# Kernel tuning notes

Measured on AMD Instinct MI355X. Metric: run time of the kernel, lower is better.

Reference implementation:

```python
import jax, jax.numpy as jnp
import numpy as np

N = 100000      # nodes
E = 1600000     # edges
G = 256         # graphs in batch
D_IN = 92
D = 64          # out_dim
EPS = 1e-5      # batchnorm eps


def setup_inputs() -> dict:
    key = jax.random.key(0)
    ks = jax.random.split(key, 20)

    def lin_w(k, fan_in, fan_out):
        return jax.random.normal(k, (fan_in, fan_out), jnp.float32) / np.sqrt(fan_in).astype(np.float32)

    inp = {
        "x": jax.random.normal(ks[0], (N, D_IN), jnp.float32),
        "edge_index": jax.random.randint(ks[1], (2, E), 0, N, dtype=jnp.int64),
        "edge_weight": jax.random.uniform(ks[2], (E,), jnp.float32),
        "batch": jnp.sort(jax.random.randint(ks[3], (N,), 0, G, dtype=jnp.int64)),
        # GCNConv layer 0 (in_channels -> out_dim) + BatchNorm
        "W0": lin_w(ks[4], D_IN, D), "b0": jnp.zeros((D,), jnp.float32),
        "g0": jnp.ones((D,), jnp.float32), "beta0": jnp.zeros((D,), jnp.float32),
        # GCNConv layers 1,2 (out_dim -> out_dim) + BatchNorms
        "W1": lin_w(ks[5], D, D), "b1": jnp.zeros((D,), jnp.float32),
        "g1": jnp.ones((D,), jnp.float32), "beta1": jnp.zeros((D,), jnp.float32),
        "W2": lin_w(ks[6], D, D), "b2": jnp.zeros((D,), jnp.float32),
        "g2": jnp.ones((D,), jnp.float32), "beta2": jnp.zeros((D,), jnp.float32),
        # post MLP: Linear(out_dim,100) -> ReLU -> Linear(100,1)
        "Wp1": lin_w(ks[7], D, 100), "bp1": jnp.zeros((100,), jnp.float32),
        "Wp2": lin_w(ks[8], 100, 1), "bp2": jnp.zeros((1,), jnp.float32),
    }
    return inp


def reference(x, edge_index, edge_weight, batch,
              W0, b0, g0, beta0,
              W1, b1, g1, beta1,
              W2, b2, g2, beta2,
              Wp1, bp1, Wp2, bp2):
    n = x.shape[0]
    # --- gcn_norm with self-loops (fill weight 1), symmetric normalization ---
    loop = jnp.arange(n)
    row = jnp.concatenate([edge_index[0], loop])          # source nodes
    col = jnp.concatenate([edge_index[1], loop])          # target nodes
    w = jnp.concatenate([edge_weight, jnp.ones((n,), x.dtype)])
    deg = jax.ops.segment_sum(w, col, num_segments=n)
    dinv = jnp.where(deg > 0, deg ** -0.5, 0.0)
    norm = dinv[row] * w * dinv[col]                      # [E+N]

    def conv(h, W, b):
        h = h @ W                                         # [n, D]
        msg = norm[:, None] * h[row]                      # gather + scale
        return jax.ops.segment_sum(msg, col, num_segments=n) + b

    def bn(h, g, beta):  # training-mode batchnorm over node dim
        mu = h.mean(0)
        var = h.var(0)
        return (h - mu) * jax.lax.rsqrt(var + EPS) * g + beta

    h = jax.nn.relu(bn(conv(x, W0, b0), g0, beta0))
    h = jax.nn.relu(bn(conv(h, W1, b1), g1, beta1))
    h = jax.nn.relu(bn(conv(h, W2, b2), g2, beta2))

    # global_mean_pool over graph ids
    sums = jax.ops.segment_sum(h, batch, num_segments=G)
    cnt = jax.ops.segment_sum(jnp.ones((n,), h.dtype), batch, num_segments=G)
    pooled = sums / jnp.clip(cnt, 1.0)[:, None]           # [G, D]

    return jax.nn.relu(pooled @ Wp1 + bp1) @ Wp2 + bp2    # [G, 1]
```

## Files before the change

### kernel.cpp

```cpp
#include <hip/hip_runtime.h>
#include <hip/hip_bf16.h>

#define NGRAPH 256
#define BNEPS 1e-5f
#define SEGCAP 64
#define BSHIFT 9
#define BSPAN  512
#define BCAP   10240
#define BSTRIDE 16384
#define GSTAT  8192

typedef short s16x8 __attribute__((ext_vector_type(8)));
typedef float f32x4 __attribute__((ext_vector_type(4)));

__device__ __forceinline__ float bf2f(unsigned short u) {
    return __uint_as_float(((unsigned)u) << 16);
}
__device__ __forceinline__ unsigned short f2bf(float f) {
    unsigned u = __float_as_uint(f);
    unsigned r = (u + 0x7FFFu + ((u >> 16) & 1u)) >> 16;
    return (unsigned short)r;
}

__global__ __launch_bounds__(256) void k_part(const int* __restrict__ row, const int* __restrict__ col,
                                              const float* __restrict__ w,
                                              int* __restrict__ gcur,
                                              float2* __restrict__ stage, int E, int NB) {
    __shared__ int lhist[256];
    __shared__ int lbase[256];
    int tid = threadIdx.x;
    if (tid < NB) lhist[tid] = 0;
    __syncthreads();
    int c[8], lp[8];
    int base = blockIdx.x * 2048;
    #pragma unroll
    for (int k = 0; k < 8; ++k) {
        int e = base + k * 256 + tid;
        c[k] = (e < E) ? col[e] : -1;
        lp[k] = (c[k] >= 0) ? atomicAdd(&lhist[c[k] >> BSHIFT], 1) : 0;
    }
    __syncthreads();
    if (tid < NB && lhist[tid] > 0) lbase[tid] = atomicAdd(&gcur[tid], lhist[tid]);
    __syncthreads();
    #pragma unroll
    for (int k = 0; k < 8; ++k) {
        int e = base + k * 256 + tid;
        if (c[k] < 0) continue;
        int b = c[k] >> BSHIFT;
        int doff = c[k] & (BSPAN - 1);
        int src = row[e];
        float we = w[e];
        int pos = lbase[b] + lp[k];
        if (pos < BCAP)
            stage[(size_t)b * BCAP + pos] =
                make_float2(__int_as_float((doff << 17) | src), we);
    }
}

__global__ __launch_bounds__(256) void k_place(const int* __restrict__ gcur,
                                               const float2* __restrict__ stage,
                                               int* __restrict__ rowptr,
                                               int* __restrict__ cntArr,
                                               float2* __restrict__ edata, int N) {
    __shared__ int lhist[512];
    __shared__ int lexcl[512];
    __shared__ int lcur[512];
    __shared__ int lts[256];
    int b = blockIdx.x;
    int tid = threadIdx.x;
    int cnt = min(gcur[b], BCAP);
    lhist[tid] = 0; lhist[tid + 256] = 0;
    lcur[tid] = 0;  lcur[tid + 256] = 0;
    __syncthreads();
    for (int i = tid; i < cnt; i += 256) {
        unsigned u = __float_as_uint(stage[(size_t)b * BCAP + i].x);
        atomicAdd(&lhist[u >> 17], 1);
    }
    __syncthreads();
    int c0 = (lhist[2 * tid] + 7) & ~7;
    int c1 = (lhist[2 * tid + 1] + 7) & ~7;
    int tsum = c0 + c1;
    lts[tid] = tsum;
    __syncthreads();
    for (int o = 1; o < 256; o <<= 1) {
        int t = (tid >= o) ? lts[tid - o] : 0;
        __syncthreads();
        lts[tid] += t;
        __syncthreads();
    }
    int excl = lts[tid] - tsum;
    lexcl[2 * tid] = excl;
    lexcl[2 * tid + 1] = excl + c0;
    __syncthreads();
    int base = b * BSTRIDE;
    for (int i = tid; i < 512; i += 256) {
        int node = (b << BSHIFT) + i;
        if (node < N) { rowptr[node] = base + lexcl[i]; cntArr[node] = lhist[i]; }
    }
    for (int i = tid; i < cnt; i += 256) {
        float2 p = stage[(size_t)b * BCAP + i];
        unsigned u = __float_as_uint(p.x);
        int doff = (int)(u >> 17);
        int src  = (int)(u & 0x1FFFFu);
        int lp = atomicAdd(&lcur[doff], 1);
        int pos = lexcl[doff] + lp;
        if (pos < BSTRIDE)
            edata[(size_t)base + pos] = make_float2(__int_as_float(src), p.y);
    }
    __syncthreads();
    for (int i = tid; i < 512; i += 256) {
        int c = lhist[i];
        int e8 = (c + 7) & ~7;
        int st = lexcl[i];
        for (int j = c; j < e8; ++j) {
            int pos = st + j;
            if (pos < BSTRIDE) edata[(size_t)base + pos] = make_float2(0.0f, 0.0f);
        }
    }
}

__global__ __launch_bounds__(256) void k_deg(const int* __restrict__ rowptr,
                                             const int* __restrict__ cntArr,
                                             const float2* __restrict__ edata,
                                             float* __restrict__ dinv, int n) {
    int node = (blockIdx.x * 256 + threadIdx.x) >> 6;
    int lane = threadIdx.x & 63;
    if (node >= n) return;
    int cnt = min(cntArr[node], SEGCAP);
    const float2* seg = edata + rowptr[node];
    float v = (lane < cnt) ? seg[lane].y : 0.0f;
    #pragma unroll
    for (int o = 32; o > 0; o >>= 1) v += __shfl_xor(v, o, 64);
    if (lane == 0) dinv[node] = rsqrtf(1.0f + v);
}

template<int K, bool FUSE_BN>
__global__ __launch_bounds__(256) void k_gemm_m(const float* __restrict__ Hin,
                                                const float* __restrict__ W,
                                                const float* __restrict__ stats,
                                                const float* __restrict__ g,
                                                const float* __restrict__ beta,
                                                const float* __restrict__ dinv,
                                                unsigned short* __restrict__ H2b, int n, float inv_n) {
    constexpr int KP = (K + 31) & ~31;
    constexpr int PITCH = KP + 8;
    __shared__ unsigned short lX[64 * PITCH];
    __shared__ unsigned short lWt[64 * PITCH];
    __shared__ float lmu[64], lsc[64], lbe[64], ldv[64];
    int tid = threadIdx.x;
    int base = blockIdx.x * 64;
    if (FUSE_BN) {
        if (tid < 64) {
            float mu  = stats[tid] * inv_n;
            float var = stats[64 + tid] * inv_n - mu * mu;
            lmu[tid] = mu;
            lsc[tid] = g[tid] * rsqrtf(var + BNEPS);
            lbe[tid] = beta[tid];
        }
        __syncthreads();
    }
    if (tid < 64) {
        int node = base + tid;
        ldv[tid] = (node < n) ? dinv[node] : 0.0f;
    }
    constexpr int XF4 = K / 4;
    for (int idx = tid; idx < 64 * XF4; idx += 256) {
        int nl = idx / XF4;
        int k4 = (idx - nl * XF4) * 4;
        int node = base + nl;
        float4 v = make_float4(0.0f, 0.0f, 0.0f, 0.0f);
        if (node < n) v = *(const float4*)&Hin[(size_t)node * K + k4];
        if (FUSE_BN) {
            v.x = fmaxf((v.x - lmu[k4 + 0]) * lsc[k4 + 0] + lbe[k4 + 0], 0.0f);
            v.y = fmaxf((v.y - lmu[k4 + 1]) * lsc[k4 + 1] + lbe[k4 + 1], 0.0f);
            v.z = fmaxf((v.z - lmu[k4 + 2]) * lsc[k4 + 2] + lbe[k4 + 2], 0.0f);
            v.w = fmaxf((v.w - lmu[k4 + 3]) * lsc[k4 + 3] + lbe[k4 + 3], 0.0f);
        }
        ushort4 pk;
        pk.x = f2bf(v.x); pk.y = f2bf(v.y); pk.z = f2bf(v.z); pk.w = f2bf(v.w);
        *(ushort4*)&lX[nl * PITCH + k4] = pk;
    }
    if constexpr (KP > K) {
        for (int idx = tid; idx < 64 * (KP - K); idx += 256) {
            int nl = idx / (KP - K);
            int kk = K + idx - nl * (KP - K);
            lX[nl * PITCH + kk] = 0;
        }
    }
    for (int idx = tid; idx < K * 16; idx += 256) {
        int kk = idx >> 4;
        int d4 = (idx & 15) * 4;
        float4 v = *(const float4*)&W[(size_t)kk * 64 + d4];
        lWt[(d4 + 0) * PITCH + kk] = f2bf(v.x);
        lWt[(d4 + 1) * PITCH + kk] = f2bf(v.y);
        lWt[(d4 + 2) * PITCH + kk] = f2bf(v.z);
        lWt[(d4 + 3) * PITCH + kk] = f2bf(v.w);
    }
    if constexpr (KP > K) {
        for (int idx = tid; idx < 64 * (KP - K); idx += 256) {
            int dl = idx / (KP - K);
            int kk = K + idx - dl * (KP - K);
            lWt[dl * PITCH + kk] = 0;
        }
    }
    __syncthreads();

    int w = tid >> 6, lane = tid & 63;
    int lrow = lane & 15, kb = lane >> 4;
    f32x4 acc0 = {0.0f, 0.0f, 0.0f, 0.0f};
    f32x4 acc1 = {0.0f, 0.0f, 0.0f, 0.0f};
    f32x4 acc2 = {0.0f, 0.0f, 0.0f, 0.0f};
    f32x4 acc3 = {0.0f, 0.0f, 0.0f, 0.0f};
    #pragma unroll
    for (int k0 = 0; k0 < KP; k0 += 32) {
        int ko = k0 + kb * 8;
        s16x8 a  = *(const s16x8*)&lX[(w * 16 + lrow) * PITCH + ko];
        s16x8 b0 = *(const s16x8*)&lWt[(0  + lrow) * PITCH + ko];
        s16x8 b1 = *(const s16x8*)&lWt[(16 + lrow) * PITCH + ko];
        s16x8 b2 = *(const s16x8*)&lWt[(32 + lrow) * PITCH + ko];
        s16x8 b3 = *(const s16x8*)&lWt[(48 + lrow) * PITCH + ko];
        acc0 = __builtin_amdgcn_mfma_f32_16x16x32_bf16(a, b0, acc0, 0, 0, 0);
        acc1 = __builtin_amdgcn_mfma_f32_16x16x32_bf16(a, b1, acc1, 0, 0, 0);
        acc2 = __builtin_amdgcn_mfma_f32_16x16x32_bf16(a, b2, acc2, 0, 0, 0);
        acc3 = __builtin_amdgcn_mfma_f32_16x16x32_bf16(a, b3, acc3, 0, 0, 0);
    }
    int nrow0 = w * 16 + kb * 4;
    #pragma unroll
    for (int r = 0; r < 4; ++r) {
        int node = base + nrow0 + r;
        if (node < n) {
            float dv = ldv[nrow0 + r];
            size_t rb = (size_t)node * 64;
            H2b[rb + 0  + lrow] = f2bf(acc0[r] * dv);
            H2b[rb + 16 + lrow] = f2bf(acc1[r] * dv);
            H2b[rb + 32 + lrow] = f2bf(acc2[r] * dv);
            H2b[rb + 48 + lrow] = f2bf(acc3[r] * dv);
        }
    }
}

__global__ __launch_bounds__(256) void k_gather(const int* __restrict__ rowptr,
                                                const int* __restrict__ cntArr,
                                                const float2* __restrict__ edata,
                                                const unsigned short* __restrict__ Hb,
                                                const float* __restrict__ b,
                                                const float* __restrict__ dinv,
                                                float* __restrict__ AGG,
                                                float* __restrict__ part, int n, int G) {
    int lane = threadIdx.x & 63;
    int half = lane >> 5;
    unsigned d2 = (unsigned)(lane & 31) * 2;
    int wid = blockIdx.x * 4 + (threadIdx.x >> 6);
    float sx = 0.0f, sy = 0.0f, qx = 0.0f, qy = 0.0f;

    for (int node = wid; node < n; node += G * 4) {
        int cnt = min(cntArr[node], SEGCAP);
        int e8 = (cnt + 7) & ~7;
        const float2* segh = edata + rowptr[node] + half;
        float ax = 0.0f, ay = 0.0f;
        int p = 0;
        for (; p + 16 <= e8; p += 16) {
            float2 e0 = segh[p];
            float2 e1 = segh[p + 2];
            float2 e2 = segh[p + 4];
            float2 e3 = segh[p + 6];
            float2 e4 = segh[p + 8];
            float2 e5 = segh[p + 10];
            float2 e6 = segh[p + 12];
            float2 e7 = segh[p + 14];
            unsigned o0 = (((unsigned)__float_as_int(e0.x)) << 6) + d2;
            unsigned o1 = (((unsigned)__float_as_int(e1.x)) << 6) + d2;
            unsigned o2 = (((unsigned)__float_as_int(e2.x)) << 6) + d2;
            unsigned o3 = (((unsigned)__float_as_int(e3.x)) << 6) + d2;
            unsigned o4 = (((unsigned)__float_as_int(e4.x)) << 6) + d2;
            unsigned o5 = (((unsigned)__float_as_int(e5.x)) << 6) + d2;
            unsigned o6 = (((unsigned)__float_as_int(e6.x)) << 6) + d2;
            unsigned o7 = (((unsigned)__float_as_int(e7.x)) << 6) + d2;
            unsigned u0 = *(const unsigned*)&Hb[o0];
            unsigned u1 = *(const unsigned*)&Hb[o1];
            unsigned u2 = *(const unsigned*)&Hb[o2];
            unsigned u3 = *(const unsigned*)&Hb[o3];
            unsigned u4 = *(const unsigned*)&Hb[o4];
            unsigned u5 = *(const unsigned*)&Hb[o5];
            unsigned u6 = *(const unsigned*)&Hb[o6];
            unsigned u7 = *(const unsigned*)&Hb[o7];
            ax = fmaf(e0.y, __uint_as_float(u0 << 16), ax);
            ay = fmaf(e0.y, __uint_as_float(u0 & 0xFFFF0000u), ay);
            ax = fmaf(e1.y, __uint_as_float(u1 << 16), ax);
            ay = fmaf(e1.y, __uint_as_float(u1 & 0xFFFF0000u), ay);
            ax = fmaf(e2.y, __uint_as_float(u2 << 16), ax);
            ay = fmaf(e2.y, __uint_as_float(u2 & 0xFFFF0000u), ay);
            ax = fmaf(e3.y, __uint_as_float(u3 << 16), ax);
            ay = fmaf(e3.y, __uint_as_float(u3 & 0xFFFF0000u), ay);
            ax = fmaf(e4.y, __uint_as_float(u4 << 16), ax);
            ay = fmaf(e4.y, __uint_as_float(u4 & 0xFFFF0000u), ay);
            ax = fmaf(e5.y, __uint_as_float(u5 << 16), ax);
            ay = fmaf(e5.y, __uint_as_float(u5 & 0xFFFF0000u), ay);
            ax = fmaf(e6.y, __uint_as_float(u6 << 16), ax);
            ay = fmaf(e6.y, __uint_as_float(u6 & 0xFFFF0000u), ay);
            ax = fmaf(e7.y, __uint_as_float(u7 << 16), ax);
            ay = fmaf(e7.y, __uint_as_float(u7 & 0xFFFF0000u), ay);
        }
        if (p < e8) {
            float2 e0 = segh[p];
            float2 e1 = segh[p + 2];
            float2 e2 = segh[p + 4];
            float2 e3 = segh[p + 6];
            unsigned o0 = (((unsigned)__float_as_int(e0.x)) << 6) + d2;
            unsigned o1 = (((unsigned)__float_as_int(e1.x)) << 6) + d2;
            unsigned o2 = (((unsigned)__float_as_int(e2.x)) << 6) + d2;
            unsigned o3 = (((unsigned)__float_as_int(e3.x)) << 6) + d2;
            unsigned u0 = *(const unsigned*)&Hb[o0];
            unsigned u1 = *(const unsigned*)&Hb[o1];
            unsigned u2 = *(const unsigned*)&Hb[o2];
            unsigned u3 = *(const unsigned*)&Hb[o3];
            ax = fmaf(e0.y, __uint_as_float(u0 << 16), ax);
            ay = fmaf(e0.y, __uint_as_float(u0 & 0xFFFF0000u), ay);
            ax = fmaf(e1.y, __uint_as_float(u1 << 16), ax);
            ay = fmaf(e1.y, __uint_as_float(u1 & 0xFFFF0000u), ay);
            ax = fmaf(e2.y, __uint_as_float(u2 << 16), ax);
            ay = fmaf(e2.y, __uint_as_float(u2 & 0xFFFF0000u), ay);
            ax = fmaf(e3.y, __uint_as_float(u3 << 16), ax);
            ay = fmaf(e3.y, __uint_as_float(u3 & 0xFFFF0000u), ay);
        }
        ax += __shfl_xor(ax, 32, 64);
        ay += __shfl_xor(ay, 32, 64);
        if (half == 0) {
            unsigned us = *(const unsigned*)&Hb[((unsigned)node << 6) + d2];
            ax += __uint_as_float(us << 16);
            ay += __uint_as_float(us & 0xFFFF0000u);
            float dv = dinv[node];
            float2 bb = *(const float2*)&b[d2];
            float2 r;
            r.x = fmaf(dv, ax, bb.x);
            r.y = fmaf(dv, ay, bb.y);
            *(float2*)&AGG[((size_t)node << 6) + d2] = r;
            sx += r.x; sy += r.y;
            qx = fmaf(r.x, r.x, qx); qy = fmaf(r.y, r.y, qy);
        }
    }

    __shared__ float lred[4][64];
    __shared__ float lq[4][64];
    int w = threadIdx.x >> 6;
    if (half == 0) {
        lred[w][d2] = sx; lred[w][d2 + 1] = sy;
        lq[w][d2] = qx;   lq[w][d2 + 1] = qy;
    }
    __syncthreads();
    if (threadIdx.x < 64) {
        int j = threadIdx.x;
        float s = lred[0][j] + lred[1][j] + lred[2][j] + lred[3][j];
        float q = lq[0][j] + lq[1][j] + lq[2][j] + lq[3][j];
        size_t pb = (size_t)blockIdx.x * 128;
        part[pb + j] = s;
        part[pb + 64 + j] = q;
    }
}

__global__ __launch_bounds__(256) void k_red(const float* __restrict__ part,
                                             float* __restrict__ stats, int G) {
    int s = blockIdx.x;
    float v = 0.0f;
    for (int t = threadIdx.x; t < G; t += 256) v += part[(size_t)t * 128 + s];
    __shared__ float l[256];
    l[threadIdx.x] = v;
    __syncthreads();
    for (int o = 128; o > 0; o >>= 1) {
        if (threadIdx.x < o) l[threadIdx.x] += l[threadIdx.x + o];
        __syncthreads();
    }
    if (threadIdx.x == 0) stats[s] = l[0];
}

__global__ __launch_bounds__(256) void k_pool_mlp(const float* __restrict__ AGG,
                                                  const float* __restrict__ stats,
                                                  const float* __restrict__ g,
                                                  const float* __restrict__ beta,
                                                  const int* __restrict__ batch, int n,
                                                  const float* __restrict__ Wp1,
                                                  const float* __restrict__ bp1,
                                                  const float* __restrict__ Wp2,
                                                  const float* __restrict__ bp2,
                                                  float* __restrict__ out, float inv_n) {
    __shared__ float lmu[64], lsc[64], lbe[64];
    int j = threadIdx.x;
    if (j < 64) {
        float mu  = stats[j] * inv_n;
        float var = stats[64 + j] * inv_n - mu * mu;
        lmu[j] = mu;
        lsc[j] = g[j] * rsqrtf(var + BNEPS);
        lbe[j] = beta[j];
    }
    __syncthreads();

    int gidx = blockIdx.x;
    int lo = 0, hi = n;
    while (lo < hi) { int mid = (lo + hi) >> 1; if (batch[mid] < gidx) lo = mid + 1; else hi = mid; }
    int start = lo;
    lo = start; hi = n;
    while (lo < hi) { int mid = (lo + hi) >> 1; if (batch[mid] < gidx + 1) lo = mid + 1; else hi = mid; }
    int end = lo;

    int d = threadIdx.x & 63, grp = threadIdx.x >> 6;
    float s = 0.0f;
    for (int r = start + grp; r < end; r += 4) {
        float v = AGG[(size_t)r * 64 + d];
        s += fmaxf((v - lmu[d]) * lsc[d] + lbe[d], 0.0f);
    }
    __shared__ float ls[256];
    __shared__ float pooled[64];
    ls[threadIdx.x] = s;
    __syncthreads();
    if (grp == 0) {
        float cnt = (float)(end - start);
        float denom = fmaxf(cnt, 1.0f);
        pooled[d] = (ls[d] + ls[64 + d] + ls[128 + d] + ls[192 + d]) / denom;
    }
    __syncthreads();
    __shared__ float hidden[100];
    if (j < 100) {
        float h = bp1[j];
        #pragma unroll 8
        for (int dd = 0; dd < 64; ++dd) h += pooled[dd] * Wp1[dd * 100 + j];
        hidden[j] = fmaxf(h, 0.0f);
    }
    __syncthreads();
    __shared__ float red[256];
    red[j] = (j < 100) ? hidden[j] * Wp2[j] : 0.0f;
    __syncthreads();
    for (int sft = 128; sft > 0; sft >>= 1) {
        if (j < sft) red[j] += red[j + sft];
        __syncthreads();
    }
    if (j == 0) out[gidx] = red[0] + bp2[0];
}

extern "C" void kernel_launch(void* const* d_in, const int* in_sizes, int n_in,
                              void* d_out, int out_size, void* d_ws, size_t ws_size,
                              hipStream_t stream) {
    const float* x    = (const float*)d_in[0];
    const int*   eidx = (const int*)d_in[1];
    const float* ew   = (const float*)d_in[2];
    const int*   batch= (const int*)d_in[3];
    const float* W0 = (const float*)d_in[4];  const float* b0 = (const float*)d_in[5];
    const float* g0 = (const float*)d_in[6];  const float* be0= (const float*)d_in[7];
    const float* W1 = (const float*)d_in[8];  const float* b1 = (const float*)d_in[9];
    const float* g1 = (const float*)d_in[10]; const float* be1= (const float*)d_in[11];
    const float* W2 = (const float*)d_in[12]; const float* b2 = (const float*)d_in[13];
    const float* g2 = (const float*)d_in[14]; const float* be2= (const float*)d_in[15];
    const float* Wp1= (const float*)d_in[16]; const float* bp1= (const float*)d_in[17];
    const float* Wp2= (const float*)d_in[18]; const float* bp2= (const float*)d_in[19];
    float* out = (float*)d_out;

    const int N = in_sizes[3];
    const int E = in_sizes[2];
    const int* row = eidx;
    const int* col = eidx + E;
    const int NB = (N + BSPAN - 1) >> BSHIFT;

    size_t off = 0;
    auto alloc = [&](size_t bytes) {
        void* p = (char*)d_ws + off;
        off += (bytes + 255) & ~(size_t)255;
        return p;
    };
    int*    rowptr = (int*)alloc((size_t)N * 4);
    int*    cntArr = (int*)alloc((size_t)N * 4);
    int*    gcur   = (int*)alloc((size_t)NB * 4);
    float*  dinv   = (float*)alloc((size_t)N * 4);
    float2* stage  = (float2*)alloc((size_t)NB * BCAP * 8);
    float2* edata  = (float2*)alloc((size_t)NB * BSTRIDE * 8);
    unsigned short* H2b = (unsigned short*)alloc((size_t)N * 64 * 2);
    float*  AGG    = (float*)alloc((size_t)N * 64 * 4);
    float*  part   = (float*)alloc((size_t)128 * GSTAT * 4);
    float*  stats  = (float*)alloc(512);
    (void)ws_size;

    const int TB = 256;
    const int gPart = (E + 2047) / 2048;
    const int gGemm = (N + 63) / 64;
    const int gDeg  = (N + 3) / 4;
    const float inv_n = 1.0f / (float)N;

    hipMemsetAsync(gcur, 0, (size_t)NB * 4, stream);
    k_part<<<gPart, TB, 0, stream>>>(row, col, ew, gcur, stage, E, NB);
    k_place<<<NB, TB, 0, stream>>>(gcur, stage, rowptr, cntArr, edata, N);
    k_deg<<<gDeg, TB, 0, stream>>>(rowptr, cntArr, edata, dinv, N);

    k_gemm_m<92, false><<<gGemm, TB, 0, stream>>>(x, W0, nullptr, nullptr, nullptr, dinv, H2b, N, inv_n);
    k_gather<<<GSTAT, TB, 0, stream>>>(rowptr, cntArr, edata, H2b, b0, dinv, AGG, part, N, GSTAT);
    k_red<<<128, TB, 0, stream>>>(part, stats, GSTAT);

    k_gemm_m<64, true><<<gGemm, TB, 0, stream>>>(AGG, W1, stats, g0, be0, dinv, H2b, N, inv_n);
    k_gather<<<GSTAT, TB, 0, stream>>>(rowptr, cntArr, edata, H2b, b1, dinv, AGG, part, N, GSTAT);
    k_red<<<128, TB, 0, stream>>>(part, stats, GSTAT);

    k_gemm_m<64, true><<<gGemm, TB, 0, stream>>>(AGG, W2, stats, g1, be1, dinv, H2b, N, inv_n);
    k_gather<<<GSTAT, TB, 0, stream>>>(rowptr, cntArr, edata, H2b, b2, dinv, AGG, part, N, GSTAT);
    k_red<<<128, TB, 0, stream>>>(part, stats, GSTAT);

    k_pool_mlp<<<NGRAPH, TB, 0, stream>>>(AGG, stats, g2, be2, batch, N,
                                          Wp1, bp1, Wp2, bp2, out, inv_n);

    (void)n_in; (void)out_size;
}
```

Before: 354.4 us.

## Fuse degree computation into placement and interleave two nodes per wave in gather

The degree/dinv computation moves into k_place, which now sums edge weights per destination with shared-memory atomics, so the separate k_deg launch and its re-read of edata go away. The gather kernel now processes two nodes per wavefront and interleaves their 8-edge units, so more independent loads are in flight and the per-node tail imbalance shrinks. In exchange, the degree sum now uses float atomics, whose order is not deterministic, and the gather uses more registers and a different loop structure.

```diff
diff --git a/kernel.cpp b/kernel.cpp
--- a/kernel.cpp
+++ b/kernel.cpp
@@ -61,16 +61,19 @@
                                                const float2* __restrict__ stage,
                                                int* __restrict__ rowptr,
                                                int* __restrict__ cntArr,
-                                               float2* __restrict__ edata, int N) {
+                                               float2* __restrict__ edata,
+                                               float* __restrict__ dinv, int N) {
     __shared__ int lhist[512];
     __shared__ int lexcl[512];
     __shared__ int lcur[512];
+    __shared__ float lwsum[512];
     __shared__ int lts[256];
     int b = blockIdx.x;
     int tid = threadIdx.x;
     int cnt = min(gcur[b], BCAP);
     lhist[tid] = 0; lhist[tid + 256] = 0;
     lcur[tid] = 0;  lcur[tid + 256] = 0;
+    lwsum[tid] = 0.0f; lwsum[tid + 256] = 0.0f;
     __syncthreads();
     for (int i = tid; i < cnt; i += 256) {
         unsigned u = __float_as_uint(stage[(size_t)b * BCAP + i].x);
@@ -103,12 +106,15 @@
         int doff = (int)(u >> 17);
         int src  = (int)(u & 0x1FFFFu);
         int lp = atomicAdd(&lcur[doff], 1);
+        atomicAdd(&lwsum[doff], p.y);
         int pos = lexcl[doff] + lp;
         if (pos < BSTRIDE)
             edata[(size_t)base + pos] = make_float2(__int_as_float(src), p.y);
     }
     __syncthreads();
     for (int i = tid; i < 512; i += 256) {
+        int node = (b << BSHIFT) + i;
+        if (node < N) dinv[node] = rsqrtf(1.0f + lwsum[i]);
         int c = lhist[i];
         int e8 = (c + 7) & ~7;
         int st = lexcl[i];
@@ -117,21 +123,6 @@
             if (pos < BSTRIDE) edata[(size_t)base + pos] = make_float2(0.0f, 0.0f);
         }
     }
-}
-
-__global__ __launch_bounds__(256) void k_deg(const int* __restrict__ rowptr,
-                                             const int* __restrict__ cntArr,
-                                             const float2* __restrict__ edata,
-                                             float* __restrict__ dinv, int n) {
-    int node = (blockIdx.x * 256 + threadIdx.x) >> 6;
-    int lane = threadIdx.x & 63;
-    if (node >= n) return;
-    int cnt = min(cntArr[node], SEGCAP);
-    const float2* seg = edata + rowptr[node];
-    float v = (lane < cnt) ? seg[lane].y : 0.0f;
-    #pragma unroll
-    for (int o = 32; o > 0; o >>= 1) v += __shfl_xor(v, o, 64);
-    if (lane == 0) dinv[node] = rsqrtf(1.0f + v);
 }
 
 template<int K, bool FUSE_BN>
@@ -239,6 +230,31 @@
     }
 }
 
+__device__ __forceinline__ void unit8(const float2* __restrict__ segh, int p, unsigned d2,
+                                      const unsigned short* __restrict__ Hb,
+                                      float& ax, float& ay) {
+    float2 e0 = segh[p];
+    float2 e1 = segh[p + 2];
+    float2 e2 = segh[p + 4];
+    float2 e3 = segh[p + 6];
+    unsigned o0 = (((unsigned)__float_as_int(e0.x)) << 6) + d2;
+    unsigned o1 = (((unsigned)__float_as_int(e1.x)) << 6) + d2;
+    unsigned o2 = (((unsigned)__float_as_int(e2.x)) << 6) + d2;
+    unsigned o3 = (((unsigned)__float_as_int(e3.x)) << 6) + d2;
+    unsigned u0 = *(const unsigned*)&Hb[o0];
+    unsigned u1 = *(const unsigned*)&Hb[o1];
+    unsigned u2 = *(const unsigned*)&Hb[o2];
+    unsigned u3 = *(const unsigned*)&Hb[o3];
+    ax = fmaf(e0.y, __uint_as_float(u0 << 16), ax);
+    ay = fmaf(e0.y, __uint_as_float(u0 & 0xFFFF0000u), ay);
+    ax = fmaf(e1.y, __uint_as_float(u1 << 16), ax);
+    ay = fmaf(e1.y, __uint_as_float(u1 & 0xFFFF0000u), ay);
+    ax = fmaf(e2.y, __uint_as_float(u2 << 16), ax);
+    ay = fmaf(e2.y, __uint_as_float(u2 & 0xFFFF0000u), ay);
+    ax = fmaf(e3.y, __uint_as_float(u3 << 16), ax);
+    ay = fmaf(e3.y, __uint_as_float(u3 & 0xFFFF0000u), ay);
+}
+
 __global__ __launch_bounds__(256) void k_gather(const int* __restrict__ rowptr,
                                                 const int* __restrict__ cntArr,
                                                 const float2* __restrict__ edata,
@@ -253,90 +269,55 @@
     int wid = blockIdx.x * 4 + (threadIdx.x >> 6);
     float sx = 0.0f, sy = 0.0f, qx = 0.0f, qy = 0.0f;
 
-    for (int node = wid; node < n; node += G * 4) {
-        int cnt = min(cntArr[node], SEGCAP);
-        int e8 = (cnt + 7) & ~7;
-        const float2* segh = edata + rowptr[node] + half;
-        float ax = 0.0f, ay = 0.0f;
-        int p = 0;
-        for (; p + 16 <= e8; p += 16) {
-            float2 e0 = segh[p];
-            float2 e1 = segh[p + 2];
-            float2 e2 = segh[p + 4];
-            float2 e3 = segh[p + 6];
-            float2 e4 = segh[p + 8];
-            float2 e5 = segh[p + 10];
-            float2 e6 = segh[p + 12];
-            float2 e7 = segh[p + 14];
-            unsigned o0 = (((unsigned)__float_as_int(e0.x)) << 6) + d2;
-            unsigned o1 = (((unsigned)__float_as_int(e1.x)) << 6) + d2;
-            unsigned o2 = (((unsigned)__float_as_int(e2.x)) << 6) + d2;
-            unsigned o3 = (((unsigned)__float_as_int(e3.x)) << 6) + d2;
-            unsigned o4 = (((unsigned)__float_as_int(e4.x)) << 6) + d2;
-            unsigned o5 = (((unsigned)__float_as_int(e5.x)) << 6) + d2;
-            unsigned o6 = (((unsigned)__float_as_int(e6.x)) << 6) + d2;
-            unsigned o7 = (((unsigned)__float_as_int(e7.x)) << 6) + d2;
-            unsigned u0 = *(const unsigned*)&Hb[o0];
-            unsigned u1 = *(const unsigned*)&Hb[o1];
-            unsigned u2 = *(const unsigned*)&Hb[o2];
-            unsigned u3 = *(const unsigned*)&Hb[o3];
-            unsigned u4 = *(const unsigned*)&Hb[o4];
-            unsigned u5 = *(const unsigned*)&Hb[o5];
-            unsigned u6 = *(const unsigned*)&Hb[o6];
-            unsigned u7 = *(const unsigned*)&Hb[o7];
-            ax = fmaf(e0.y, __uint_as_float(u0 << 16), ax);
-            ay = fmaf(e0.y, __uint_as_float(u0 & 0xFFFF0000u), ay);
-            ax = fmaf(e1.y, __uint_as_float(u1 << 16), ax);
-            ay = fmaf(e1.y, __uint_as_float(u1 & 0xFFFF0000u), ay);
-            ax = fmaf(e2.y, __uint_as_float(u2 << 16), ax);
-            ay = fmaf(e2.y, __uint_as_float(u2 & 0xFFFF0000u), ay);
-            ax = fmaf(e3.y, __uint_as_float(u3 << 16), ax);
-            ay = fmaf(e3.y, __uint_as_float(u3 & 0xFFFF0000u), ay);
-            ax = fmaf(e4.y, __uint_as_float(u4 << 16), ax);
-            ay = fmaf(e4.y, __uint_as_float(u4 & 0xFFFF0000u), ay);
-            ax = fmaf(e5.y, __uint_as_float(u5 << 16), ax);
-            ay = fmaf(e5.y, __uint_as_float(u5 & 0xFFFF0000u), ay);
-            ax = fmaf(e6.y, __uint_as_float(u6 << 16), ax);
-            ay = fmaf(e6.y, __uint_as_float(u6 & 0xFFFF0000u), ay);
-            ax = fmaf(e7.y, __uint_as_float(u7 << 16), ax);
-            ay = fmaf(e7.y, __uint_as_float(u7 & 0xFFFF0000u), ay);
-        }
-        if (p < e8) {
-            float2 e0 = segh[p];
-            float2 e1 = segh[p + 2];
-            float2 e2 = segh[p + 4];
-            float2 e3 = segh[p + 6];
-            unsigned o0 = (((unsigned)__float_as_int(e0.x)) << 6) + d2;
-            unsigned o1 = (((unsigned)__float_as_int(e1.x)) << 6) + d2;
-            unsigned o2 = (((unsigned)__float_as_int(e2.x)) << 6) + d2;
-            unsigned o3 = (((unsigned)__float_as_int(e3.x)) << 6) + d2;
-            unsigned u0 = *(const unsigned*)&Hb[o0];
-            unsigned u1 = *(const unsigned*)&Hb[o1];
-            unsigned u2 = *(const unsigned*)&Hb[o2];
-            unsigned u3 = *(const unsigned*)&Hb[o3];
-            ax = fmaf(e0.y, __uint_as_float(u0 << 16), ax);
-            ay = fmaf(e0.y, __uint_as_float(u0 & 0xFFFF0000u), ay);
-            ax = fmaf(e1.y, __uint_as_float(u1 << 16), ax);
-            ay = fmaf(e1.y, __uint_as_float(u1 & 0xFFFF0000u), ay);
-            ax = fmaf(e2.y, __uint_as_float(u2 << 16), ax);
-            ay = fmaf(e2.y, __uint_as_float(u2 & 0xFFFF0000u), ay);
-            ax = fmaf(e3.y, __uint_as_float(u3 << 16), ax);
-            ay = fmaf(e3.y, __uint_as_float(u3 & 0xFFFF0000u), ay);
-        }
-        ax += __shfl_xor(ax, 32, 64);
-        ay += __shfl_xor(ay, 32, 64);
+    for (int nA = wid * 2; nA < n; nA += G * 8) {
+        int nB = nA + 1;
+        bool hasB = (nB < n);
+        int e8A = ((min(cntArr[nA], SEGCAP) + 7) & ~7);
+        int e8B = hasB ? ((min(cntArr[nB], SEGCAP) + 7) & ~7) : 0;
+        const float2* shA = edata + rowptr[nA] + half;
+        const float2* shB = hasB ? (edata + rowptr[nB] + half) : shA;
+        float axA = 0.0f, ayA = 0.0f, axB = 0.0f, ayB = 0.0f;
+        int uA = e8A >> 3, uB = e8B >> 3;
+        int uc = min(uA, uB);
+        int pA = 0, pB = 0;
+        for (int t = 0; t < uc; ++t) {
+            unit8(shA, pA, d2, Hb, axA, ayA); pA += 8;
+            unit8(shB, pB, d2, Hb, axB, ayB); pB += 8;
+        }
+        for (; pA < e8A; pA += 8) unit8(shA, pA, d2, Hb, axA, ayA);
+        for (; pB < e8B; pB += 8) unit8(shB, pB, d2, Hb, axB, ayB);
+
+        axA += __shfl_xor(axA, 32, 64);
+        ayA += __shfl_xor(ayA, 32, 64);
+        axB += __shfl_xor(axB, 32, 64);
+        ayB += __shfl_xor(ayB, 32, 64);
         if (half == 0) {
-            unsigned us = *(const unsigned*)&Hb[((unsigned)node << 6) + d2];
-            ax += __uint_as_float(us << 16);
-            ay += __uint_as_float(us & 0xFFFF0000u);
-            float dv = dinv[node];
-            float2 bb = *(const float2*)&b[d2];
-            float2 r;
-            r.x = fmaf(dv, ax, bb.x);
-            r.y = fmaf(dv, ay, bb.y);
-            *(float2*)&AGG[((size_t)node << 6) + d2] = r;
-            sx += r.x; sy += r.y;
-            qx = fmaf(r.x, r.x, qx); qy = fmaf(r.y, r.y, qy);
+            {
+                unsigned us = *(const unsigned*)&Hb[((unsigned)nA << 6) + d2];
+                float ax = axA + __uint_as_float(us << 16);
+                float ay = ayA + __uint_as_float(us & 0xFFFF0000u);
+                float dv = dinv[nA];
+                float2 bb = *(const float2*)&b[d2];
+                float2 r;
+                r.x = fmaf(dv, ax, bb.x);
+                r.y = fmaf(dv, ay, bb.y);
+                *(float2*)&AGG[((size_t)nA << 6) + d2] = r;
+                sx += r.x; sy += r.y;
+                qx = fmaf(r.x, r.x, qx); qy = fmaf(r.y, r.y, qy);
+            }
+            if (hasB) {
+                unsigned us = *(const unsigned*)&Hb[((unsigned)nB << 6) + d2];
+                float ax = axB + __uint_as_float(us << 16);
+                float ay = ayB + __uint_as_float(us & 0xFFFF0000u);
+                float dv = dinv[nB];
+                float2 bb = *(const float2*)&b[d2];
+                float2 r;
+                r.x = fmaf(dv, ax, bb.x);
+                r.y = fmaf(dv, ay, bb.y);
+                *(float2*)&AGG[((size_t)nB << 6) + d2] = r;
+                sx += r.x; sy += r.y;
+                qx = fmaf(r.x, r.x, qx); qy = fmaf(r.y, r.y, qy);
+            }
         }
     }
 
@@ -480,13 +461,11 @@
     const int TB = 256;
     const int gPart = (E + 2047) / 2048;
     const int gGemm = (N + 63) / 64;
-    const int gDeg  = (N + 3) / 4;
     const float inv_n = 1.0f / (float)N;
 
     hipMemsetAsync(gcur, 0, (size_t)NB * 4, stream);
     k_part<<<gPart, TB, 0, stream>>>(row, col, ew, gcur, stage, E, NB);
-    k_place<<<NB, TB, 0, stream>>>(gcur, stage, rowptr, cntArr, edata, N);
-    k_deg<<<gDeg, TB, 0, stream>>>(rowptr, cntArr, edata, dinv, N);
+    k_place<<<NB, TB, 0, stream>>>(gcur, stage, rowptr, cntArr, edata, dinv, N);
 
     k_gemm_m<92, false><<<gGemm, TB, 0, stream>>>(x, W0, nullptr, nullptr, nullptr, dinv, H2b, N, inv_n);
     k_gather<<<GSTAT, TB, 0, stream>>>(rowptr, cntArr, edata, H2b, b0, dinv, AGG, part, N, GSTAT);
```

Measured after the change: 332.0 us. 6.3% less time.
